# Performance work log

Hardware: AMD Instinct MI355X
Metric: run time of the kernel (lower is better)

## Reference

```python
import jax, jax.numpy as jnp
import numpy as np
from jax import lax

POINTS = 512  # number of FPS-sampled centroids
KNN = 16      # neighbors per centroid


def setup_inputs() -> dict:
    key = jax.random.key(0)
    # [B, N, 3+C]: first 3 channels are xyz coordinates, rest are features
    x = jax.random.normal(key, (8, 16384, 16), dtype=jnp.float32)
    return {"x": x}


def _furthest_point_sample(xyz, npoint):
    """Standard FPS (seeded at index 0, as in the pointnet2 CUDA op).
    xyz: [B, N, 3] -> idx: [B, npoint] int32."""
    B, N, _ = xyz.shape

    def step(carry, _):
        min_d, last = carry
        last_pt = jnp.take_along_axis(xyz, last[:, None, None], axis=1)  # [B,1,3]
        d = jnp.sum((xyz - last_pt) ** 2, axis=-1)                        # [B,N]
        min_d = jnp.minimum(min_d, d)
        nxt = jnp.argmax(min_d, axis=-1).astype(jnp.int32)
        return (min_d, nxt), nxt

    first = jnp.zeros((B,), dtype=jnp.int32)
    init = (jnp.full((B, N), 1e10, dtype=xyz.dtype), first)
    _, rest = lax.scan(step, init, None, length=npoint - 1)  # [npoint-1, B]
    return jnp.concatenate([first[:, None], rest.T], axis=1)  # [B, npoint]


def _index_points(points, idx):
    """points: [B,N,C], idx: [B,S] or [B,S,K] -> gathered [*idx.shape, C]."""
    B = points.shape[0]
    flat = idx.reshape(B, -1)                                  # [B, S*K]
    out = jnp.take_along_axis(points, flat[:, :, None], axis=1)
    return out.reshape(*idx.shape, points.shape[-1])


def reference(x):
    # FPS over coordinates only
    idx = _furthest_point_sample(x[:, :, :3], POINTS)          # [B, P]
    sampled = _index_points(x, idx)                             # [B, P, 3+C]
    s = sampled[:, :, :3]
    p = x[:, :, :3]
    # squared euclidean distance: ||s||^2 + ||p||^2 - 2 s.p  -> [B, P, N]
    dist = (jnp.sum(s * s, axis=-1)[:, :, None]
            + jnp.sum(p * p, axis=-1)[:, None, :]
            - 2.0 * jnp.einsum('bpc,bnc->bpn', s, p))
    # full argsort then slice, matching distances.argsort()[:, :, :knn]
    knn_idx = jnp.argsort(dist, axis=-1)[:, :, :KNN]            # [B, P, K]
    return _index_points(x, knn_idx)                            # [B, P, K, 3+C]
```

## Files before the change

### kernel.cpp

```cpp
#include <hip/hip_runtime.h>
#include <hip/hip_bf16.h>
#include <stdint.h>

#define B_      8
#define N_      16384
#define NPOINT  512
#define KNN_    16
#define C_      16

__device__ __forceinline__ float fmulrn(float a, float b){ return __fmul_rn(a,b); }
__device__ __forceinline__ float faddrn(float a, float b){ return __fadd_rn(a,b); }
__device__ __forceinline__ float fsubrn(float a, float b){ return __fsub_rn(a,b); }

__device__ __forceinline__ uint32_t umax_(uint32_t a, uint32_t b){ return a > b ? a : b; }

__device__ __forceinline__ uint32_t row16_max(uint32_t x){
    uint32_t t;
    t = (uint32_t)__builtin_amdgcn_update_dpp((int)x, (int)x, 0x111, 0xf, 0xf, false); x = umax_(x, t);
    t = (uint32_t)__builtin_amdgcn_update_dpp((int)x, (int)x, 0x112, 0xf, 0xf, false); x = umax_(x, t);
    t = (uint32_t)__builtin_amdgcn_update_dpp((int)x, (int)x, 0x114, 0xf, 0xf, false); x = umax_(x, t);
    t = (uint32_t)__builtin_amdgcn_update_dpp((int)x, (int)x, 0x118, 0xf, 0xf, false); x = umax_(x, t);
    return x;
}

__device__ __forceinline__ uint32_t wave_max_uniform(uint32_t x){
    x = row16_max(x);
    uint32_t a = (uint32_t)__builtin_amdgcn_readlane((int)x, 15);
    uint32_t b = (uint32_t)__builtin_amdgcn_readlane((int)x, 31);
    uint32_t c = (uint32_t)__builtin_amdgcn_readlane((int)x, 47);
    uint32_t d = (uint32_t)__builtin_amdgcn_readlane((int)x, 63);
    return umax_(umax_(a, b), umax_(c, d));
}

__global__ void prep_kernel(const float* __restrict__ x, float4* __restrict__ pts){
    int i = blockIdx.x * blockDim.x + threadIdx.x;
    if (i >= B_ * N_) return;
    const float4* x4 = (const float4*)x;
    float4 q = x4[(size_t)i * 4];
    float p2 = faddrn(faddrn(fmulrn(q.x,q.x), fmulrn(q.y,q.y)), fmulrn(q.z,q.z));
    pts[i] = make_float4(q.x, q.y, q.z, p2);
}

#define FPS_T   1024
#define FPS_NW  (FPS_T/64)
#define FPS_LDS_BYTES (N_ * 2 * (int)sizeof(float))

#define FOR_SLOTS(F) F(0) F(1) F(2) F(3) F(4) F(5) F(6) F(7) \
                     F(8) F(9) F(10) F(11) F(12) F(13) F(14) F(15)

__global__ void __launch_bounds__(FPS_T)
__attribute__((amdgpu_waves_per_eu(4, 4)))
fps_kernel(const float4* __restrict__ pts, float4* __restrict__ s_out){
    extern __shared__ float2 xy[];
    __shared__ uint32_t red_v[2][FPS_NW];
    __shared__ uint32_t red_i[2][FPS_NW];

    const int b    = blockIdx.x;
    const int tid  = threadIdx.x;
    const int lane = tid & 63;
    const int wv   = tid >> 6;
    const float4* P = pts + (size_t)b * N_;

#define DECL_SLOT(s) float z##s, md##s;
    FOR_SLOTS(DECL_SLOT)
#undef DECL_SLOT

#define INIT_SLOT(s) { float4 q = P[(s) * FPS_T + tid]; \
        xy[(s) * FPS_T + tid] = make_float2(q.x, q.y); \
        z##s = q.z; md##s = 1e10f; }
    FOR_SLOTS(INIT_SLOT)
#undef INIT_SLOT

    float lx, ly, lz;
    {
        float4 q0 = P[0];
        lx = q0.x; ly = q0.y; lz = q0.z;
        if (tid == 0) s_out[(size_t)b * NPOINT + 0] = q0;
    }
    __syncthreads();

    for (int it = 1; it < NPOINT; ++it){
        float    bv = -1.0f;
        uint32_t bi = 0;
#define DO_SLOT(s) { \
        float2 c = xy[(s) * FPS_T + tid]; \
        float dx = fsubrn(c.x, lx); \
        float dy = fsubrn(c.y, ly); \
        float dz = fsubrn(z##s, lz); \
        float d  = faddrn(faddrn(fmulrn(dx,dx), fmulrn(dy,dy)), fmulrn(dz,dz)); \
        md##s = fminf(md##s, d); \
        if (md##s > bv){ bv = md##s; bi = (uint32_t)((s) * FPS_T + tid); } }
        FOR_SLOTS(DO_SLOT)
#undef DO_SLOT

        uint32_t vb    = __float_as_uint(bv);
        uint32_t gmaxw = wave_max_uniform(vb);
        uint32_t gidxw = wave_max_uniform((vb == gmaxw) ? ~bi : 0u);
        const int par = it & 1;
        if (lane == 0){ red_v[par][wv] = gmaxw; red_i[par][wv] = gidxw; }
        __syncthreads();
        uint32_t rv = red_v[par][lane & 15];
        uint32_t ri = red_i[par][lane & 15];
        uint32_t gv = (uint32_t)__builtin_amdgcn_readlane((int)row16_max(rv), 15);
        uint32_t gn = (uint32_t)__builtin_amdgcn_readlane(
                          (int)row16_max((rv == gv) ? ri : 0u), 15);
        uint32_t gi = ~gn;
        float4 q = P[gi];
        lx = q.x; ly = q.y; lz = q.z;
        if (tid == 0) s_out[(size_t)b * NPOINT + it] = q;
    }
}

#define FOR_V(F) F(0) F(1) F(2) F(3) F(4) F(5) F(6) F(7) \
                 F(8) F(9) F(10) F(11) F(12) F(13) F(14) F(15)

__global__ void __launch_bounds__(256)
__attribute__((amdgpu_waves_per_eu(4, 4)))
knn_kernel(const float* __restrict__ x,
           const float4* __restrict__ pts,
           const float4* __restrict__ s_arr,
           float* __restrict__ out){
    const int wv   = threadIdx.x >> 6;
    const int lane = threadIdx.x & 63;
    const int blk  = blockIdx.x;
    const int b    = blk >> 7;
    const int p    = ((blk & 127) << 2) | wv;

    const float4 s = s_arr[(size_t)b * NPOINT + p];
    const float sx = s.x, sy = s.y, sz = s.z, s2 = s.w;
    const float4* P = pts + (size_t)b * N_;

#define DECLV(t) unsigned long long v##t = ~0ULL;
    FOR_V(DECLV)
#undef DECLV

#define PROC(q, n) { \
        float dot = faddrn(faddrn(fmulrn(sz, (q).z), fmulrn(sy, (q).y)), fmulrn(sx, (q).x)); \
        float d = fsubrn(faddrn(s2, (q).w), fmulrn(2.0f, dot)); \
        uint32_t bits = __float_as_uint(d); \
        uint32_t key  = bits ^ (((uint32_t)((int32_t)bits >> 31)) | 0x80000000u); \
        unsigned long long c = ((unsigned long long)key << 32) | (uint32_t)(n); \
        if (c < v15){ \
            INS(0) INS(1) INS(2) INS(3) INS(4) INS(5) INS(6) INS(7) \
            INS(8) INS(9) INS(10) INS(11) INS(12) INS(13) INS(14) INS(15) \
        } }
#define INS(t) { bool lt = c < v##t; \
                 unsigned long long lo = lt ? c : v##t; \
                 unsigned long long hi = lt ? v##t : c; \
                 v##t = lo; c = hi; }

    #pragma unroll 1
    for (int j = 0; j < N_/64; j += 4){
        const int n0 = (j << 6) | lane;
        float4 q0 = P[n0];
        float4 q1 = P[n0 + 64];
        float4 q2 = P[n0 + 128];
        float4 q3 = P[n0 + 192];
        PROC(q0, n0)
        PROC(q1, n0 + 64)
        PROC(q2, n0 + 128)
        PROC(q3, n0 + 192)
    }
#undef INS
#undef PROC

    uint32_t myidx = 0;
    const int myr = lane >> 2;
    #pragma unroll 1
    for (int r = 0; r < KNN_; ++r){
        unsigned long long h = v0;
        unsigned long long g = h;
        #pragma unroll
        for (int off = 1; off < 64; off <<= 1){
            unsigned long long o = __shfl_xor(g, off, 64);
            if (o < g) g = o;
        }
        if (h == g){
            v0=v1; v1=v2; v2=v3; v3=v4; v4=v5; v5=v6; v6=v7; v7=v8;
            v8=v9; v9=v10; v10=v11; v11=v12; v12=v13; v13=v14; v14=v15;
            v15=~0ULL;
        }
        if (myr == r) myidx = (uint32_t)g;
    }

    const int c4 = lane & 3;
    const float4* X4 = (const float4*)x;
    float4 valq = X4[((size_t)b * N_ + myidx) * 4 + c4];
    float4* O4 = (float4*)out;
    O4[(((size_t)b * NPOINT + p) * KNN_ + myr) * 4 + c4] = valq;
}

extern "C" void kernel_launch(void* const* d_in, const int* in_sizes, int n_in,
                              void* d_out, int out_size, void* d_ws, size_t ws_size,
                              hipStream_t stream) {
    const float* x = (const float*)d_in[0];
    float* out = (float*)d_out;

    const size_t pts_bytes = (size_t)B_ * N_ * sizeof(float4);
    const size_t s_bytes   = (size_t)B_ * NPOINT * sizeof(float4);
    if (ws_size < pts_bytes + s_bytes) return;
    float4* pts   = (float4*)d_ws;
    float4* s_arr = (float4*)((char*)d_ws + pts_bytes);

    prep_kernel<<<(B_*N_ + 255)/256, 256, 0, stream>>>(x, pts);
    fps_kernel<<<B_, FPS_T, FPS_LDS_BYTES, stream>>>(pts, s_arr);
    knn_kernel<<<(B_*NPOINT)/4, 256, 0, stream>>>(x, pts, s_arr, out);
}
```

Baseline: 1.116 ms.

## Split FPS across four blocks per batch with global-memory mailbox reduction

Each batch's furthest-point sampling now runs on four workgroups, each owning a quarter of the points. They exchange per-iteration (max distance, index) keys through atomic stores and polling loads on a zeroed global mailbox, then each reduces the four keys locally. The aim is to use more CUs for the serial FPS loop and cut per-thread work from 16 slots to 4. The cost is a cross-block spin-wait every iteration, plus a risk of deadlock if the 32 blocks are not all resident at once, which a guard counter only partly covers.

```diff
diff --git a/kernel.cpp b/kernel.cpp
--- a/kernel.cpp
+++ b/kernel.cpp
@@ -32,6 +32,23 @@
     return umax_(umax_(a, b), umax_(c, d));
 }
 
+__device__ __forceinline__ unsigned long long quad_max_u64(unsigned long long k){
+    uint32_t lo = (uint32_t)k, hi = (uint32_t)(k >> 32);
+    {
+        uint32_t olo = (uint32_t)__builtin_amdgcn_update_dpp((int)lo, (int)lo, 0xB1, 0xf, 0xf, false);
+        uint32_t ohi = (uint32_t)__builtin_amdgcn_update_dpp((int)hi, (int)hi, 0xB1, 0xf, 0xf, false);
+        bool take = (ohi > hi) || (ohi == hi && olo > lo);
+        hi = take ? ohi : hi; lo = take ? olo : lo;
+    }
+    {
+        uint32_t olo = (uint32_t)__builtin_amdgcn_update_dpp((int)lo, (int)lo, 0x4E, 0xf, 0xf, false);
+        uint32_t ohi = (uint32_t)__builtin_amdgcn_update_dpp((int)hi, (int)hi, 0x4E, 0xf, 0xf, false);
+        bool take = (ohi > hi) || (ohi == hi && olo > lo);
+        hi = take ? ohi : hi; lo = take ? olo : lo;
+    }
+    return ((unsigned long long)hi << 32) | lo;
+}
+
 __global__ void prep_kernel(const float* __restrict__ x, float4* __restrict__ pts){
     int i = blockIdx.x * blockDim.x + threadIdx.x;
     if (i >= B_ * N_) return;
@@ -41,57 +58,66 @@
     pts[i] = make_float4(q.x, q.y, q.z, p2);
 }
 
-#define FPS_T   1024
-#define FPS_NW  (FPS_T/64)
-#define FPS_LDS_BYTES (N_ * 2 * (int)sizeof(float))
-
-#define FOR_SLOTS(F) F(0) F(1) F(2) F(3) F(4) F(5) F(6) F(7) \
-                     F(8) F(9) F(10) F(11) F(12) F(13) F(14) F(15)
+#define FPS_NB  4
+__global__ void zero_part_kernel(unsigned long long* __restrict__ part){
+    int i = blockIdx.x * blockDim.x + threadIdx.x;
+    if (i < B_ * NPOINT * FPS_NB) part[i] = 0ULL;
+}
+
+#define FPS_T    1024
+#define FPS_NW   (FPS_T/64)
+#define SLICE    (N_ / FPS_NB)
+#define SLOTS_MB (SLICE / FPS_T)
+
+#define FOR_S4(F) F(0) F(1) F(2) F(3)
 
 __global__ void __launch_bounds__(FPS_T)
-__attribute__((amdgpu_waves_per_eu(4, 4)))
-fps_kernel(const float4* __restrict__ pts, float4* __restrict__ s_out){
-    extern __shared__ float2 xy[];
+fps_kernel_mb(const float4* __restrict__ pts, float4* __restrict__ s_out,
+              unsigned long long* __restrict__ part){
+    __shared__ float2   xy[SLICE];
     __shared__ uint32_t red_v[2][FPS_NW];
     __shared__ uint32_t red_i[2][FPS_NW];
 
-    const int b    = blockIdx.x;
+    const int b    = blockIdx.x & 7;
+    const int blk  = blockIdx.x >> 3;
     const int tid  = threadIdx.x;
     const int lane = tid & 63;
     const int wv   = tid >> 6;
+    const int base = blk * SLICE;
     const float4* P = pts + (size_t)b * N_;
-
-#define DECL_SLOT(s) float z##s, md##s;
-    FOR_SLOTS(DECL_SLOT)
-#undef DECL_SLOT
-
-#define INIT_SLOT(s) { float4 q = P[(s) * FPS_T + tid]; \
+    unsigned long long* mbox = part + ((size_t)b * NPOINT) * FPS_NB;
+
+#define DECL_S(s) float z##s, md##s;
+    FOR_S4(DECL_S)
+#undef DECL_S
+
+#define INIT_S(s) { float4 q = P[base + (s) * FPS_T + tid]; \
         xy[(s) * FPS_T + tid] = make_float2(q.x, q.y); \
         z##s = q.z; md##s = 1e10f; }
-    FOR_SLOTS(INIT_SLOT)
-#undef INIT_SLOT
+    FOR_S4(INIT_S)
+#undef INIT_S
 
     float lx, ly, lz;
     {
         float4 q0 = P[0];
         lx = q0.x; ly = q0.y; lz = q0.z;
-        if (tid == 0) s_out[(size_t)b * NPOINT + 0] = q0;
+        if (blk == 0 && tid == 0) s_out[(size_t)b * NPOINT + 0] = q0;
     }
     __syncthreads();
 
     for (int it = 1; it < NPOINT; ++it){
         float    bv = -1.0f;
         uint32_t bi = 0;
-#define DO_SLOT(s) { \
+#define DO_S(s) { \
         float2 c = xy[(s) * FPS_T + tid]; \
         float dx = fsubrn(c.x, lx); \
         float dy = fsubrn(c.y, ly); \
         float dz = fsubrn(z##s, lz); \
         float d  = faddrn(faddrn(fmulrn(dx,dx), fmulrn(dy,dy)), fmulrn(dz,dz)); \
         md##s = fminf(md##s, d); \
-        if (md##s > bv){ bv = md##s; bi = (uint32_t)((s) * FPS_T + tid); } }
-        FOR_SLOTS(DO_SLOT)
-#undef DO_SLOT
+        if (md##s > bv){ bv = md##s; bi = (uint32_t)(base + (s) * FPS_T + tid); } }
+        FOR_S4(DO_S)
+#undef DO_S
 
         uint32_t vb    = __float_as_uint(bv);
         uint32_t gmaxw = wave_max_uniform(vb);
@@ -104,10 +130,27 @@
         uint32_t gv = (uint32_t)__builtin_amdgcn_readlane((int)row16_max(rv), 15);
         uint32_t gn = (uint32_t)__builtin_amdgcn_readlane(
                           (int)row16_max((rv == gv) ? ri : 0u), 15);
-        uint32_t gi = ~gn;
-        float4 q = P[gi];
+        unsigned long long kblk = ((unsigned long long)gv << 32) | gn;
+
+        unsigned long long* slotp = mbox + (size_t)it * FPS_NB;
+        if (tid == 0)
+            __hip_atomic_store(&slotp[blk], kblk, __ATOMIC_RELAXED,
+                               __HIP_MEMORY_SCOPE_AGENT);
+        unsigned long long v = 0;
+        int guard = 0;
+        for (;;){
+            if (v == 0)
+                v = __hip_atomic_load(&slotp[lane & 3], __ATOMIC_RELAXED,
+                                      __HIP_MEMORY_SCOPE_AGENT);
+            if (__all(v != 0ULL)) break;
+            if (++guard > (1 << 20)) return;
+        }
+        unsigned long long kmax = quad_max_u64(v);
+        uint32_t gi  = ~((uint32_t)kmax);
+        uint32_t giu = (uint32_t)__builtin_amdgcn_readfirstlane((int)gi);
+        float4 q = P[giu];
         lx = q.x; ly = q.y; lz = q.z;
-        if (tid == 0) s_out[(size_t)b * NPOINT + it] = q;
+        if (blk == 0 && tid == 0) s_out[(size_t)b * NPOINT + it] = q;
     }
 }
 
@@ -196,13 +239,17 @@
     const float* x = (const float*)d_in[0];
     float* out = (float*)d_out;
 
-    const size_t pts_bytes = (size_t)B_ * N_ * sizeof(float4);
-    const size_t s_bytes   = (size_t)B_ * NPOINT * sizeof(float4);
-    if (ws_size < pts_bytes + s_bytes) return;
+    const size_t pts_bytes  = (size_t)B_ * N_ * sizeof(float4);
+    const size_t s_bytes    = (size_t)B_ * NPOINT * sizeof(float4);
+    const size_t part_bytes = (size_t)B_ * NPOINT * FPS_NB * sizeof(unsigned long long);
+    if (ws_size < pts_bytes + s_bytes + part_bytes) return;
     float4* pts   = (float4*)d_ws;
     float4* s_arr = (float4*)((char*)d_ws + pts_bytes);
+    unsigned long long* part =
+        (unsigned long long*)((char*)d_ws + pts_bytes + s_bytes);
 
     prep_kernel<<<(B_*N_ + 255)/256, 256, 0, stream>>>(x, pts);
-    fps_kernel<<<B_, FPS_T, FPS_LDS_BYTES, stream>>>(pts, s_arr);
+    zero_part_kernel<<<(B_*NPOINT*FPS_NB + 255)/256, 256, 0, stream>>>(part);
+    fps_kernel_mb<<<B_*FPS_NB, FPS_T, 0, stream>>>(pts, s_arr, part);
     knn_kernel<<<(B_*NPOINT)/4, 256, 0, stream>>>(x, pts, s_arr, out);
 }
```

Result: faster. 1.056 ms (-5.4%).
